# Kernel optimization log

Measured on AMD Instinct MI355X. Metric: run time of the kernel, lower is better.

The kernel has to match this reference:

```python
import jax, jax.numpy as jnp
import numpy as np

B, L, D = 16, 1024, 768

def setup_inputs() -> dict:
    key = jax.random.key(0)
    ks = jax.random.split(key, 6)
    s = 1.0 / np.sqrt(D)  # torch Linear default init scale
    return {
        "h": jax.random.normal(ks[0], (B, L, D), dtype=jnp.float32),
        "q": jax.random.normal(ks[1], (B, L, D), dtype=jnp.float32),
        "w1_w": jax.random.uniform(ks[2], (L, D), jnp.float32, -s, s),
        "w1_b": jax.random.uniform(ks[3], (L,), jnp.float32, -s, s),
        "w2_w": jax.random.uniform(ks[4], (L, D), jnp.float32, -s, s),
        "w2_b": jax.random.uniform(ks[5], (L,), jnp.float32, -s, s),
    }

def reference(h, q, w1_w, w1_b, w2_w, w2_b):
    # w1h: [B, L, l], w2q: [B, L, l] -> permuted [B, l, L]
    w1h = jnp.einsum('bsd,ld->bsl', h, w1_w) + w1_b
    w2q = jnp.einsum('btd,ld->btl', q, w2_w) + w2_b
    w3hq = jnp.einsum('bsd,btd->bst', h, q)           # [B, L, L]
    a = w1h + jnp.swapaxes(w2q, 1, 2) + w3hq          # [B, L, L]
    p = jax.nn.softmax(a, axis=2)
    c = jnp.einsum('bst,btd->bsd', p, q)              # [B, L, D]
    m = jnp.max(a, axis=2)                            # [B, L]
    p2 = jax.nn.softmax(m, axis=1)                    # [B, L]
    qc = h * p2[:, :, None]                           # [B, L, D]
    return jnp.concatenate([h, c, h * c, qc * c], axis=2)  # [B, L, 4D]
```

## Files before the change

kernel.cpp:

```cpp
#include <hip/hip_runtime.h>
#include <stdint.h>

#define B_  16
#define L_  1024
#define D_  768
#define K1_ 1536

typedef unsigned short u16;
typedef __attribute__((ext_vector_type(4))) float f32x4;
typedef __attribute__((ext_vector_type(8))) _Float16 f16x8;

__device__ __forceinline__ u16 f2h(float x){
    return __builtin_bit_cast(u16, (_Float16)x);
}

__device__ __forceinline__ void gload_lds16(const void* g, void* l){
    __builtin_amdgcn_global_load_lds((const __attribute__((address_space(1))) void*)g,
                                     (__attribute__((address_space(3))) void*)l, 16, 0, 0);
}

__global__ __launch_bounds__(256) void prep(const float* __restrict__ h, const float* __restrict__ q,
    const float* __restrict__ w1w, const float* __restrict__ w2w,
    u16* __restrict__ hH, u16* __restrict__ wH, u16* __restrict__ qH,
    u16* __restrict__ w1h, u16* __restrict__ qT, int b0, int nb)
{
    __shared__ float tile[32][33];
    int bb = blockIdx.z, bg = b0 + bb;
    int t0 = blockIdx.x * 32, d0 = blockIdx.y * 32;
    int tid = threadIdx.x;
    int r  = tid >> 3;
    int c4 = (tid & 7) * 4;
    int t = t0 + r, d = d0 + c4;
    size_t goff = (size_t)t * D_ + d;

    float4 qv  = *(const float4*)(q   + (size_t)bg * L_ * D_ + goff);
    float4 hv  = *(const float4*)(h   + (size_t)bg * L_ * D_ + goff);
    float4 w2v = *(const float4*)(w2w + goff);

    tile[r][c4 + 0] = qv.x; tile[r][c4 + 1] = qv.y;
    tile[r][c4 + 2] = qv.z; tile[r][c4 + 3] = qv.w;

    size_t o = ((size_t)bb * L_ + t) * D_ + d;
    ushort4 a;
    a.x = f2h(hv.x); a.y = f2h(hv.y); a.z = f2h(hv.z); a.w = f2h(hv.w);
    *(ushort4*)(hH + o) = a;
    a.x = f2h(hv.x + w2v.x); a.y = f2h(hv.y + w2v.y);
    a.z = f2h(hv.z + w2v.z); a.w = f2h(hv.w + w2v.w);
    *(ushort4*)(wH + o) = a;
    a.x = f2h(qv.x); a.y = f2h(qv.y); a.z = f2h(qv.z); a.w = f2h(qv.w);
    *(ushort4*)(qH + o) = a;
    if (bb == 0){
        float4 w1v = *(const float4*)(w1w + goff);
        a.x = f2h(w1v.x); a.y = f2h(w1v.y); a.z = f2h(w1v.z); a.w = f2h(w1v.w);
        *(ushort4*)(w1h + goff) = a;
    }
    __syncthreads();
    int dr = tid >> 3;
    int tc = (tid & 7) * 4;
    ushort4 b;
    b.x = f2h(tile[tc + 0][dr]); b.y = f2h(tile[tc + 1][dr]);
    b.z = f2h(tile[tc + 2][dr]); b.w = f2h(tile[tc + 3][dr]);
    *(ushort4*)(qT + (size_t)bb * D_ * L_ + (size_t)(d0 + dr) * L_ + t0 + tc) = b;
}

__global__ __launch_bounds__(512) void gemm1(
    const u16* __restrict__ hH, const u16* __restrict__ wH,
    const u16* __restrict__ qH, const u16* __restrict__ w1h,
    const float* __restrict__ w1b, const float* __restrict__ w2b,
    u16* __restrict__ pT, float* __restrict__ mT, float* __restrict__ sT)
{
    __shared__ u16 ldsA[2][256 * 64];
    __shared__ u16 ldsB[2][256 * 64];
    int nwg = gridDim.x;
    int o = blockIdx.x;
    int wg = (o & 7) * (nwg >> 3) + (o >> 3);
    int bb = wg >> 4;
    int tl = wg & 15;
    int smb = tl >> 2, tnb = tl & 3;
    int s0 = smb * 256, t0 = tnb * 256;
    int tid = threadIdx.x;
    int lane = tid & 63, wid = tid >> 6;
    int wm2 = wid >> 2, wn2 = wid & 3;
    int l15 = lane & 15, l4 = lane >> 4;

    const u16* hHb = hH + (size_t)bb * L_ * D_;
    const u16* wHb = wH + (size_t)bb * L_ * D_;
    const u16* qHb = qH + (size_t)bb * L_ * D_;

    f32x4 acc[8][4];
    #pragma unroll
    for (int m = 0; m < 8; m++)
        #pragma unroll
        for (int n = 0; n < 4; n++)
            acc[m][n] = (f32x4){0.f, 0.f, 0.f, 0.f};

    auto stage = [&](int t){
        int kb = t * 64;
        bool inH = (kb < D_);
        const u16* As = inH ? hHb : wHb;
        const u16* Bs = inH ? w1h : qHb;
        int koff = inH ? kb : (kb - D_);
        int buf = t & 1;
        #pragma unroll
        for (int q = 0; q < 4; q++){
            int idx = q * 512 + tid;
            int row = idx >> 3, c = idx & 7;
            int cc = c ^ (row & 7);
            int dst = (q * 512 + wid * 64) * 8;
            gload_lds16(As + (size_t)(s0 + row) * D_ + koff + cc * 8, &ldsA[buf][dst]);
            gload_lds16(Bs + (size_t)(t0 + row) * D_ + koff + cc * 8, &ldsB[buf][dst]);
        }
    };

    stage(0);
    asm volatile("s_waitcnt vmcnt(0)" ::: "memory");
    __builtin_amdgcn_s_barrier();

    for (int t = 0; t < 24; t++){
        if (t + 1 < 24) stage(t + 1);
        int bsel = t & 1;
        #pragma unroll
        for (int kk = 0; kk < 2; kk++){
            f16x8 bf[4];
            #pragma unroll
            for (int n = 0; n < 4; n++){
                int row = wn2 * 64 + n * 16 + l15;
                int c = kk * 4 + l4;
                bf[n] = *(const f16x8*)&ldsB[bsel][(row * 8 + (c ^ (row & 7))) * 8];
            }
            #pragma unroll
            for (int mh = 0; mh < 2; mh++){
                f16x8 af[4];
                #pragma unroll
                for (int mi = 0; mi < 4; mi++){
                    int row = wm2 * 128 + (mh * 4 + mi) * 16 + l15;
                    int c = kk * 4 + l4;
                    af[mi] = *(const f16x8*)&ldsA[bsel][(row * 8 + (c ^ (row & 7))) * 8];
                }
                __builtin_amdgcn_s_setprio(1);
                #pragma unroll
                for (int mi = 0; mi < 4; mi++)
                    #pragma unroll
                    for (int n = 0; n < 4; n++)
                        acc[mh * 4 + mi][n] = __builtin_amdgcn_mfma_f32_16x16x32_f16(
                            af[mi], bf[n], acc[mh * 4 + mi][n], 0, 0, 0);
                __builtin_amdgcn_s_setprio(0);
            }
        }
        asm volatile("s_waitcnt vmcnt(0)" ::: "memory");
        __builtin_amdgcn_s_barrier();
    }

    u16* pRow = pT + (size_t)bb * L_ * L_;
    #pragma unroll
    for (int m = 0; m < 8; m++){
        #pragma unroll
        for (int r = 0; r < 4; r++){
            int s = s0 + wm2 * 128 + m * 16 + l4 * 4 + r;
            float w2v = w2b[s];
            float v[4];
            float tmax = -1e30f;
            #pragma unroll
            for (int n = 0; n < 4; n++){
                int tcol = t0 + wn2 * 64 + n * 16 + l15;
                v[n] = acc[m][n][r] + w1b[tcol] + w2v;
                tmax = fmaxf(tmax, v[n]);
            }
            #pragma unroll
            for (int o2 = 1; o2 < 16; o2 <<= 1)
                tmax = fmaxf(tmax, __shfl_xor(tmax, o2));
            float e[4];
            float gsum = 0.f;
            #pragma unroll
            for (int n = 0; n < 4; n++){
                e[n] = __expf(v[n] - tmax);
                gsum += e[n];
            }
            #pragma unroll
            for (int n = 0; n < 4; n++){
                int tcol = t0 + wn2 * 64 + n * 16 + l15;
                pRow[(size_t)s * L_ + tcol] = f2h(e[n]);
            }
            #pragma unroll
            for (int o2 = 1; o2 < 16; o2 <<= 1)
                gsum += __shfl_xor(gsum, o2);
            if (l15 == 0){
                size_t mo = ((size_t)bb * L_ + s) * 16 + tnb * 4 + wn2;
                mT[mo] = tmax;
                sT[mo] = gsum;
            }
        }
    }
}

__global__ __launch_bounds__(1024) void p2k(const float* __restrict__ mT, const float* __restrict__ sT,
                                            float* __restrict__ p2, float* __restrict__ sc, int b0)
{
    __shared__ float red[16];
    int bb = blockIdx.x, bg = b0 + bb;
    int tid = threadIdx.x;
    const float4* mv = (const float4*)(mT + ((size_t)bb * L_ + tid) * 16);
    float4 m0 = mv[0], m1 = mv[1], m2 = mv[2], m3 = mv[3];
    float mj[16] = {m0.x, m0.y, m0.z, m0.w, m1.x, m1.y, m1.z, m1.w,
                    m2.x, m2.y, m2.z, m2.w, m3.x, m3.y, m3.z, m3.w};
    float v = mj[0];
    #pragma unroll
    for (int i = 1; i < 16; i++) v = fmaxf(v, mj[i]);

    float mx = v;
    #pragma unroll
    for (int o = 32; o; o >>= 1) mx = fmaxf(mx, __shfl_xor(mx, o));
    if ((tid & 63) == 0) red[tid >> 6] = mx;
    __syncthreads();
    float m2g = red[0];
    #pragma unroll
    for (int i = 1; i < 16; i++) m2g = fmaxf(m2g, red[i]);
    float e = __expf(v - m2g);
    float sum = e;
    #pragma unroll
    for (int o = 32; o; o >>= 1) sum += __shfl_xor(sum, o);
    __syncthreads();
    if ((tid & 63) == 0) red[tid >> 6] = sum;
    __syncthreads();
    float st = 0.f;
    #pragma unroll
    for (int i = 0; i < 16; i++) st += red[i];
    p2[(size_t)bg * L_ + tid] = e / st;

    const float4* sv = (const float4*)(sT + ((size_t)bb * L_ + tid) * 16);
    float4 s0v = sv[0], s1v = sv[1], s2v = sv[2], s3v = sv[3];
    float sj[16] = {s0v.x, s0v.y, s0v.z, s0v.w, s1v.x, s1v.y, s1v.z, s1v.w,
                    s2v.x, s2v.y, s2v.z, s2v.w, s3v.x, s3v.y, s3v.z, s3v.w};
    float ej[16];
    float S = 0.f;
    #pragma unroll
    for (int j = 0; j < 16; j++){
        ej[j] = __expf(mj[j] - v);
        S += sj[j] * ej[j];
    }
    float invS = 1.0f / S;
    float* scb = sc + (size_t)bb * 16 * L_;
    #pragma unroll
    for (int j = 0; j < 16; j++)
        scb[j * L_ + tid] = ej[j] * invS;
}

__global__ __launch_bounds__(256) void gemm2(const u16* __restrict__ pT, const u16* __restrict__ qT,
    const float* __restrict__ sc, float* __restrict__ out, int b0)
{
    __shared__ u16 ldsA[128 * 64];
    __shared__ u16 ldsB[128 * 64];
    int nwg = gridDim.x;
    int o = blockIdx.x;
    int wg = (o & 7) * (nwg >> 3) + (o >> 3);
    int bb = wg / 48;
    int tl = wg % 48;
    int sm = tl / 6, dn = tl % 6;
    int s0 = sm * 128, d0 = dn * 128;
    int tid = threadIdx.x;
    int lane = tid & 63, wid = tid >> 6;
    int wm = wid >> 1, wn = wid & 1;
    int l15 = lane & 15, l4 = lane >> 4;

    const u16* Ab = pT + (size_t)bb * L_ * L_;
    const u16* Bb = qT + (size_t)bb * D_ * L_;
    const float* scb = sc + (size_t)bb * 16 * L_;

    f32x4 acc[4][4];
    #pragma unroll
    for (int m = 0; m < 4; m++)
        #pragma unroll
        for (int n = 0; n < 4; n++)
            acc[m][n] = (f32x4){0.f, 0.f, 0.f, 0.f};

    for (int kb = 0; kb < L_; kb += 64){
        int jg = kb >> 6;
        #pragma unroll
        for (int j = 0; j < 4; j++){
            int n = j * 256 + tid;
            int row = n >> 3, c = n & 7;
            int cc = c ^ (row & 7);
            gload_lds16(Ab + (size_t)(s0 + row) * L_ + kb + cc * 8, &ldsA[(j * 256 + wid * 64) * 8]);
        }
        #pragma unroll
        for (int j = 0; j < 4; j++){
            int n = j * 256 + tid;
            int row = n >> 3, c = n & 7;
            int cc = c ^ (row & 7);
            gload_lds16(Bb + (size_t)(d0 + row) * L_ + kb + cc * 8, &ldsB[(j * 256 + wid * 64) * 8]);
        }
        _Float16 sch[4];
        #pragma unroll
        for (int m = 0; m < 4; m++)
            sch[m] = (_Float16)scb[(size_t)jg * L_ + s0 + wm * 64 + m * 16 + l15];
        __syncthreads();
        #pragma unroll
        for (int kk = 0; kk < 2; kk++){
            f16x8 af[4], bf[4];
            #pragma unroll
            for (int m = 0; m < 4; m++){
                int row = wm * 64 + m * 16 + l15;
                int c = kk * 4 + l4;
                af[m] = *(const f16x8*)&ldsA[(row * 8 + (c ^ (row & 7))) * 8];
                af[m] = af[m] * sch[m];
            }
            #pragma unroll
            for (int n = 0; n < 4; n++){
                int row = wn * 64 + n * 16 + l15;
                int c = kk * 4 + l4;
                bf[n] = *(const f16x8*)&ldsB[(row * 8 + (c ^ (row & 7))) * 8];
            }
            #pragma unroll
            for (int m = 0; m < 4; m++)
                #pragma unroll
                for (int n = 0; n < 4; n++)
                    acc[m][n] = __builtin_amdgcn_mfma_f32_16x16x32_f16(af[m], bf[n], acc[m][n], 0, 0, 0);
        }
        __syncthreads();
    }

    float* oC = out + ((size_t)(b0 + bb) * L_) * (4 * D_) + D_;
    #pragma unroll
    for (int m = 0; m < 4; m++){
        int sbase = s0 + wm * 64 + m * 16 + l4 * 4;
        #pragma unroll
        for (int r = 0; r < 4; r++){
            int s = sbase + r;
            #pragma unroll
            for (int n = 0; n < 4; n++){
                int d = d0 + wn * 64 + n * 16 + l15;
                oC[(size_t)s * (4 * D_) + d] = acc[m][n][r];
            }
        }
    }
}

__global__ __launch_bounds__(192) void epi(const float* __restrict__ h,
    const float* __restrict__ p2, float* __restrict__ out, int b0)
{
    int rowid = blockIdx.x;
    int bb = rowid >> 10, s = rowid & 1023;
    int bg = b0 + bb;
    float p2v = p2[(size_t)bg * L_ + s];
    const float* hR = h + ((size_t)bg * L_ + s) * D_;
    float* oR = out + ((size_t)bg * L_ + s) * (4 * D_);
    int d = threadIdx.x * 4;
    float4 cv = *(const float4*)(oR + D_ + d);
    float4 hv = *(const float4*)(hR + d);
    float4 hc = {hv.x * cv.x, hv.y * cv.y, hv.z * cv.z, hv.w * cv.w};
    float4 qc = {p2v * hc.x, p2v * hc.y, p2v * hc.z, p2v * hc.w};
    *(float4*)(oR + d)          = hv;
    *(float4*)(oR + 2 * D_ + d) = hc;
    *(float4*)(oR + 3 * D_ + d) = qc;
}

extern "C" void kernel_launch(void* const* d_in, const int* in_sizes, int n_in,
                              void* d_out, int out_size, void* d_ws, size_t ws_size,
                              hipStream_t stream)
{
    const float* h   = (const float*)d_in[0];
    const float* q   = (const float*)d_in[1];
    const float* w1w = (const float*)d_in[2];
    const float* w1b = (const float*)d_in[3];
    const float* w2w = (const float*)d_in[4];
    const float* w2b = (const float*)d_in[5];
    float* out = (float*)d_out;

    const size_t szPlane = (size_t)L_ * D_ * 2;
    const size_t szM     = (size_t)B_ * L_ * 4;
    const size_t perB_pT = (size_t)L_ * L_ * 2;
    const size_t perB_s  = (size_t)L_ * 16 * 4;
    const size_t perB = 4 * szPlane + perB_pT + 3 * perB_s;
    const size_t fixed = szPlane + szM;

    int NB = 1;
    if (ws_size > fixed){
        size_t nbc = (ws_size - fixed) / perB;
        NB = (nbc >= 16) ? 16 : (nbc < 1 ? 1 : (int)nbc);
    }

    char* p = (char*)d_ws;
    u16*   w1h  = (u16*)p;   p += szPlane;
    float* p2   = (float*)p; p += szM;
    float* mT   = (float*)p; p += perB_s * NB;
    float* sT   = (float*)p; p += perB_s * NB;
    float* sc   = (float*)p; p += perB_s * NB;
    u16*   hH   = (u16*)p;   p += szPlane * NB;
    u16*   wH   = (u16*)p;   p += szPlane * NB;
    u16*   qH   = (u16*)p;   p += szPlane * NB;
    u16*   qT   = (u16*)p;   p += szPlane * NB;
    u16*   pT   = (u16*)p;

    for (int b0 = 0; b0 < B_; b0 += NB){
        int nb = (B_ - b0 < NB) ? (B_ - b0) : NB;
        prep  <<<dim3(32, 24, nb), 256, 0, stream>>>(h, q, w1w, w2w, hH, wH, qH, w1h, qT, b0, nb);
        gemm1 <<<dim3(16 * nb), 512, 0, stream>>>(hH, wH, qH, w1h, w1b, w2b, pT, mT, sT);
        p2k   <<<dim3(nb), 1024, 0, stream>>>(mT, sT, p2, sc, b0);
        gemm2 <<<dim3(48 * nb), 256, 0, stream>>>(pT, qT, sc, out, b0);
        epi   <<<dim3(nb * 1024), 192, 0, stream>>>(h, p2, out, b0);
    }
}
```

Baseline: 205.6 us.

## Enlarge gemm2 tiles to 256x256 with double-buffered LDS and 512 threads

```diff
diff --git a/kernel.cpp b/kernel.cpp
--- a/kernel.cpp
+++ b/kernel.cpp
@@ -245,90 +245,103 @@
         scb[j * L_ + tid] = ej[j] * invS;
 }
 
-__global__ __launch_bounds__(256) void gemm2(const u16* __restrict__ pT, const u16* __restrict__ qT,
+__global__ __launch_bounds__(512) void gemm2(const u16* __restrict__ pT, const u16* __restrict__ qT,
     const float* __restrict__ sc, float* __restrict__ out, int b0)
 {
-    __shared__ u16 ldsA[128 * 64];
-    __shared__ u16 ldsB[128 * 64];
+    __shared__ u16 ldsA[2][256 * 64];
+    __shared__ u16 ldsB[2][256 * 64];
     int nwg = gridDim.x;
     int o = blockIdx.x;
-    int wg = (o & 7) * (nwg >> 3) + (o >> 3);
-    int bb = wg / 48;
-    int tl = wg % 48;
-    int sm = tl / 6, dn = tl % 6;
-    int s0 = sm * 128, d0 = dn * 128;
+    int wg = ((nwg & 7) == 0) ? ((o & 7) * (nwg >> 3) + (o >> 3)) : o;
+    int bb = wg / 12;
+    int tl = wg % 12;
+    int smb = tl >> 2, dnb = tl & 3;
+    smb = tl / 3; dnb = tl % 3;
+    int s0 = smb * 256, d0 = dnb * 256;
     int tid = threadIdx.x;
     int lane = tid & 63, wid = tid >> 6;
-    int wm = wid >> 1, wn = wid & 1;
+    int wm2 = wid >> 2, wn2 = wid & 3;
     int l15 = lane & 15, l4 = lane >> 4;
 
     const u16* Ab = pT + (size_t)bb * L_ * L_;
     const u16* Bb = qT + (size_t)bb * D_ * L_;
     const float* scb = sc + (size_t)bb * 16 * L_;
 
-    f32x4 acc[4][4];
-    #pragma unroll
-    for (int m = 0; m < 4; m++)
+    f32x4 acc[8][4];
+    #pragma unroll
+    for (int m = 0; m < 8; m++)
         #pragma unroll
         for (int n = 0; n < 4; n++)
             acc[m][n] = (f32x4){0.f, 0.f, 0.f, 0.f};
 
-    for (int kb = 0; kb < L_; kb += 64){
-        int jg = kb >> 6;
-        #pragma unroll
-        for (int j = 0; j < 4; j++){
-            int n = j * 256 + tid;
-            int row = n >> 3, c = n & 7;
+    auto stage = [&](int t){
+        int kb = t * 64;
+        int buf = t & 1;
+        #pragma unroll
+        for (int q = 0; q < 4; q++){
+            int idx = q * 512 + tid;
+            int row = idx >> 3, c = idx & 7;
             int cc = c ^ (row & 7);
-            gload_lds16(Ab + (size_t)(s0 + row) * L_ + kb + cc * 8, &ldsA[(j * 256 + wid * 64) * 8]);
-        }
-        #pragma unroll
-        for (int j = 0; j < 4; j++){
-            int n = j * 256 + tid;
-            int row = n >> 3, c = n & 7;
-            int cc = c ^ (row & 7);
-            gload_lds16(Bb + (size_t)(d0 + row) * L_ + kb + cc * 8, &ldsB[(j * 256 + wid * 64) * 8]);
-        }
-        _Float16 sch[4];
-        #pragma unroll
-        for (int m = 0; m < 4; m++)
-            sch[m] = (_Float16)scb[(size_t)jg * L_ + s0 + wm * 64 + m * 16 + l15];
-        __syncthreads();
+            int dst = (q * 512 + wid * 64) * 8;
+            gload_lds16(Ab + (size_t)(s0 + row) * L_ + kb + cc * 8, &ldsA[buf][dst]);
+            gload_lds16(Bb + (size_t)(d0 + row) * L_ + kb + cc * 8, &ldsB[buf][dst]);
+        }
+    };
+
+    stage(0);
+    asm volatile("s_waitcnt vmcnt(0)" ::: "memory");
+    __builtin_amdgcn_s_barrier();
+
+    for (int t = 0; t < 16; t++){
+        if (t + 1 < 16) stage(t + 1);
+        int bsel = t & 1;
+        _Float16 sch[8];
+        #pragma unroll
+        for (int m = 0; m < 8; m++)
+            sch[m] = (_Float16)scb[(size_t)t * L_ + s0 + wm2 * 128 + m * 16 + l15];
         #pragma unroll
         for (int kk = 0; kk < 2; kk++){
-            f16x8 af[4], bf[4];
-            #pragma unroll
-            for (int m = 0; m < 4; m++){
-                int row = wm * 64 + m * 16 + l15;
+            f16x8 bf[4];
+            #pragma unroll
+            for (int n = 0; n < 4; n++){
+                int row = wn2 * 64 + n * 16 + l15;
                 int c = kk * 4 + l4;
-                af[m] = *(const f16x8*)&ldsA[(row * 8 + (c ^ (row & 7))) * 8];
-                af[m] = af[m] * sch[m];
-            }
-            #pragma unroll
-            for (int n = 0; n < 4; n++){
-                int row = wn * 64 + n * 16 + l15;
-                int c = kk * 4 + l4;
-                bf[n] = *(const f16x8*)&ldsB[(row * 8 + (c ^ (row & 7))) * 8];
-            }
-            #pragma unroll
-            for (int m = 0; m < 4; m++)
+                bf[n] = *(const f16x8*)&ldsB[bsel][(row * 8 + (c ^ (row & 7))) * 8];
+            }
+            #pragma unroll
+            for (int mh = 0; mh < 2; mh++){
+                f16x8 af[4];
                 #pragma unroll
-                for (int n = 0; n < 4; n++)
-                    acc[m][n] = __builtin_amdgcn_mfma_f32_16x16x32_f16(af[m], bf[n], acc[m][n], 0, 0, 0);
-        }
-        __syncthreads();
+                for (int mi = 0; mi < 4; mi++){
+                    int row = wm2 * 128 + (mh * 4 + mi) * 16 + l15;
+                    int c = kk * 4 + l4;
+                    af[mi] = *(const f16x8*)&ldsA[bsel][(row * 8 + (c ^ (row & 7))) * 8];
+                    af[mi] = af[mi] * sch[mh * 4 + mi];
+                }
+                __builtin_amdgcn_s_setprio(1);
+                #pragma unroll
+                for (int mi = 0; mi < 4; mi++)
+                    #pragma unroll
+                    for (int n = 0; n < 4; n++)
+                        acc[mh * 4 + mi][n] = __builtin_amdgcn_mfma_f32_16x16x32_f16(
+                            af[mi], bf[n], acc[mh * 4 + mi][n], 0, 0, 0);
+                __builtin_amdgcn_s_setprio(0);
+            }
+        }
+        asm volatile("s_waitcnt vmcnt(0)" ::: "memory");
+        __builtin_amdgcn_s_barrier();
     }
 
     float* oC = out + ((size_t)(b0 + bb) * L_) * (4 * D_) + D_;
     #pragma unroll
-    for (int m = 0; m < 4; m++){
-        int sbase = s0 + wm * 64 + m * 16 + l4 * 4;
+    for (int m = 0; m < 8; m++){
+        int sbase = s0 + wm2 * 128 + m * 16 + l4 * 4;
         #pragma unroll
         for (int r = 0; r < 4; r++){
             int s = sbase + r;
             #pragma unroll
             for (int n = 0; n < 4; n++){
-                int d = d0 + wn * 64 + n * 16 + l15;
+                int d = d0 + wn2 * 64 + n * 16 + l15;
                 oC[(size_t)s * (4 * D_) + d] = acc[m][n][r];
             }
         }
@@ -396,7 +409,7 @@
         prep  <<<dim3(32, 24, nb), 256, 0, stream>>>(h, q, w1w, w2w, hH, wH, qH, w1h, qT, b0, nb);
         gemm1 <<<dim3(16 * nb), 512, 0, stream>>>(hH, wH, qH, w1h, w1b, w2b, pT, mT, sT);
         p2k   <<<dim3(nb), 1024, 0, stream>>>(mT, sT, p2, sc, b0);
-        gemm2 <<<dim3(48 * nb), 256, 0, stream>>>(pT, qT, sc, out, b0);
+        gemm2 <<<dim3(12 * nb), 512, 0, stream>>>(pT, qT, sc, out, b0);
         epi   <<<dim3(nb * 1024), 192, 0, stream>>>(h, p2, out, b0);
     }
 }
```

New measurement: 202.7 us. About the same (-1.4%).
